# Performance work log

Hardware: AMD Instinct MI355X
Metric: run time of the kernel (lower is better)

The kernel has to match this reference:

```python
import jax, jax.numpy as jnp
import numpy as np

N = 50000
E = 800000
D_IN = 128
HID = 128
LAT = 64
NEG_SLOPE = 0.2


def setup_inputs() -> dict:
    key = jax.random.key(0)
    ks = jax.random.split(key, 16)
    g = lambda k, shape: jax.random.normal(k, shape, dtype=jnp.float32) * (1.0 / np.sqrt(shape[0]))
    x = jax.random.normal(ks[0], (N, D_IN), dtype=jnp.float32)
    edge_index = jax.random.randint(ks[1], (2, E), 0, N, dtype=jnp.int64)
    return {
        "x": x,
        "edge_index": edge_index,
        # lin1: Linear(D_IN, HID)
        "lin1_w": g(ks[2], (D_IN, HID)),
        "lin1_b": jnp.zeros((HID,), jnp.float32),
        # conv1: GATConv((D_IN, D_IN) -> HID), heads=1
        "w1_src": g(ks[3], (D_IN, HID)),
        "w1_dst": g(ks[4], (D_IN, HID)),
        "a1_src": g(ks[5], (HID,)),
        "a1_dst": g(ks[6], (HID,)),
        "b1": jnp.zeros((HID,), jnp.float32),
        # conv2: GATConv((HID, HID) -> LAT), heads=1
        "w2_src": g(ks[7], (HID, LAT)),
        "w2_dst": g(ks[8], (HID, LAT)),
        "a2_src": g(ks[9], (LAT,)),
        "a2_dst": g(ks[10], (LAT,)),
        "b2": jnp.zeros((LAT,), jnp.float32),
    }


def _gat_conv(x, src, dst, w_src, w_dst, a_src, a_dst, b):
    """PyG GATConv, heads=1, add_self_loops=False. x: [N, Din]."""
    n = x.shape[0]
    hs = x @ w_src                    # [N, C] messages (source transform)
    hd = x @ w_dst                    # [N, C] destination transform
    alpha_s = hs @ a_src              # [N]
    alpha_d = hd @ a_dst              # [N]
    e = jax.nn.leaky_relu(alpha_s[src] + alpha_d[dst], NEG_SLOPE)  # [E]
    # segment softmax over incoming edges per destination node
    m = jax.ops.segment_max(e, dst, num_segments=n)
    ex = jnp.exp(e - m[dst])
    denom = jax.ops.segment_sum(ex, dst, num_segments=n)
    alpha = ex / (denom[dst] + 1e-16)                              # [E]
    msg = hs[src] * alpha[:, None]                                 # [E, C]
    out = jax.ops.segment_sum(msg, dst, num_segments=n)            # [N, C]
    return out + b


def reference(x, edge_index, lin1_w, lin1_b, w1_src, w1_dst, a1_src, a1_dst, b1,
              w2_src, w2_dst, a2_src, a2_dst, b2):
    src, dst = edge_index[0], edge_index[1]
    z = _gat_conv(x, src, dst, w1_src, w1_dst, a1_src, a1_dst, b1)
    z = jax.nn.relu(z + x @ lin1_w + lin1_b)
    z = _gat_conv(z, src, dst, w2_src, w2_dst, a2_src, a2_dst, b2)
    return z
```

## Files before the change

kernel.cpp:

```cpp
#include <hip/hip_runtime.h>

static constexpr int N_NODES = 50000;
static constexpr int N_EDGES = 800000;
static constexpr int NPART = 8;
static constexpr int PART_SZ = N_NODES / NPART;

typedef __attribute__((ext_vector_type(8))) short bf16x8;
typedef __attribute__((ext_vector_type(4))) float f32x4;

__device__ __forceinline__ float bf2f(unsigned short u) {
  union { unsigned int i; float f; } v; v.i = ((unsigned int)u) << 16; return v.f;
}
__device__ __forceinline__ unsigned short f2bf(float f) {
  union { unsigned int i; float f; } v; v.f = f;
  unsigned int r = (v.i + 0x7fffu + ((v.i >> 16) & 1u)) >> 16;
  return (unsigned short)r;
}
__device__ __forceinline__ int clampN(int v) {
  unsigned u = (unsigned)v; return (u < (unsigned)N_NODES) ? (int)u : 0;
}

__global__ void k_detect(const int* __restrict__ ei, int* __restrict__ flag) {
  if (threadIdx.x == 0 && blockIdx.x == 0) {
    int z = ei[1] | ei[3] | ei[5] | ei[7];
    *flag = (z == 0) ? 1 : 0;
  }
}

__global__ void k_zero_out(float* __restrict__ out, int n) {
  int i = blockIdx.x * 256 + threadIdx.x;
  if (i < n) out[i] = 0.f;
}

__global__ void k_compact(const int* __restrict__ ei, const int* __restrict__ flag,
                          int* __restrict__ s32, int* __restrict__ d32) {
  int e = blockIdx.x * 256 + threadIdx.x;
  if (e < N_EDGES) {
    int f = *flag;
    s32[e] = clampN(ei[(size_t)e << f]);
    d32[e] = clampN(ei[(size_t)(N_EDGES + e) << f]);
  }
}

__global__ void k_prepw(const float* __restrict__ w1_src, const float* __restrict__ wlin,
                        const float* __restrict__ w2_src,
                        const float* __restrict__ w1_dst, const float* __restrict__ a1_dst,
                        const float* __restrict__ w2_dst, const float* __restrict__ a2_dst,
                        unsigned short* __restrict__ w1T, unsigned short* __restrict__ w2T,
                        float* __restrict__ c1dst, float* __restrict__ c2dst) {
  int idx = blockIdx.x * 256 + threadIdx.x;
  if (idx < 256 * 128) {
    int c = idx >> 7, k = idx & 127;
    float v = (c < 128) ? w1_src[k * 128 + c] : wlin[k * 128 + (c - 128)];
    w1T[idx] = f2bf(v);
  } else if (idx < 256 * 128 + 64 * 128) {
    int r = idx - 256 * 128;
    int c = r >> 7, k = r & 127;
    w2T[r] = f2bf(w2_src[k * 64 + c]);
  } else if (blockIdx.x == 160) {
    int k = threadIdx.x;
    if (k < 128) {
      float s1 = 0.f;
      for (int c = 0; c < 128; ++c) s1 += w1_dst[k * 128 + c] * a1_dst[c];
      c1dst[k] = s1;
      float s2 = 0.f;
      for (int c = 0; c < 64; ++c) s2 += w2_dst[k * 64 + c] * a2_dst[c];
      c2dst[k] = s2;
    }
  }
}

__global__ __launch_bounds__(256) void k_gemm1(
    const float* __restrict__ x, const unsigned short* __restrict__ w1T,
    const float* __restrict__ lin_b, const float* __restrict__ a1_src,
    const float* __restrict__ c1dst,
    unsigned short* __restrict__ hs1, unsigned short* __restrict__ linzb,
    float* __restrict__ as1, float* __restrict__ ad1) {
  int tid = threadIdx.x;
  int wv = tid >> 6, l = tid & 63;
  int lrow = l & 15, lk = l >> 4;
  int nb = blockIdx.x * 64 + wv * 16;
  int rowA = nb + lrow;
  int growA = rowA < N_NODES ? rowA : N_NODES - 1;
  bf16x8 afrag[4];
  float sd = 0.f;
#pragma unroll
  for (int ks = 0; ks < 4; ++ks) {
    const float* p = x + (size_t)growA * 128 + ks * 32 + lk * 8;
    float4 a0 = *(const float4*)p;
    float4 a1 = *(const float4*)(p + 4);
    bf16x8 af;
    af[0] = (short)f2bf(a0.x); af[1] = (short)f2bf(a0.y);
    af[2] = (short)f2bf(a0.z); af[3] = (short)f2bf(a0.w);
    af[4] = (short)f2bf(a1.x); af[5] = (short)f2bf(a1.y);
    af[6] = (short)f2bf(a1.z); af[7] = (short)f2bf(a1.w);
    afrag[ks] = af;
    int k0 = ks * 32 + lk * 8;
    float4 ca = *(const float4*)(c1dst + k0);
    float4 cb = *(const float4*)(c1dst + k0 + 4);
    sd += a0.x * ca.x + a0.y * ca.y + a0.z * ca.z + a0.w * ca.w +
          a1.x * cb.x + a1.y * cb.y + a1.z * cb.z + a1.w * cb.w;
  }
  sd += __shfl_xor(sd, 16, 64);
  sd += __shfl_xor(sd, 32, 64);
  if (lk == 0 && rowA < N_NODES) ad1[rowA] = sd;

  float pa[4] = {0.f, 0.f, 0.f, 0.f};
#pragma unroll
  for (int ch = 0; ch < 4; ++ch) {
    f32x4 acc[4] = {{0.f,0.f,0.f,0.f},{0.f,0.f,0.f,0.f},{0.f,0.f,0.f,0.f},{0.f,0.f,0.f,0.f}};
#pragma unroll
    for (int ks = 0; ks < 4; ++ks) {
      bf16x8 bfrag[4];
#pragma unroll
      for (int ct = 0; ct < 4; ++ct) {
        int col = ch * 64 + ct * 16 + lrow;
        bfrag[ct] = *(const bf16x8*)(w1T + (size_t)col * 128 + ks * 32 + lk * 8);
      }
#pragma unroll
      for (int ct = 0; ct < 4; ++ct)
        acc[ct] = __builtin_amdgcn_mfma_f32_16x16x32_bf16(afrag[ks], bfrag[ct], acc[ct], 0, 0, 0);
    }
#pragma unroll
    for (int ct = 0; ct < 4; ++ct) {
      int col = ch * 64 + ct * 16 + lrow;
      float av = (col < 128) ? a1_src[col] : 0.f;
      float bb = (col < 128) ? 0.f : lin_b[col - 128];
#pragma unroll
      for (int j = 0; j < 4; ++j) {
        int row = nb + lk * 4 + j;
        float v = acc[ct][j];
        if (row < N_NODES) {
          if (col < 128) hs1[(size_t)row * 128 + col] = f2bf(v);
          else linzb[(size_t)row * 128 + (col - 128)] = f2bf(v + bb);
        }
        if (col < 128) pa[j] += v * av;
      }
    }
  }
#pragma unroll
  for (int j = 0; j < 4; ++j) {
    pa[j] += __shfl_xor(pa[j], 1, 64);
    pa[j] += __shfl_xor(pa[j], 2, 64);
    pa[j] += __shfl_xor(pa[j], 4, 64);
    pa[j] += __shfl_xor(pa[j], 8, 64);
  }
  if (lrow == 0) {
#pragma unroll
    for (int j = 0; j < 4; ++j) {
      int row = nb + lk * 4 + j;
      if (row < N_NODES) as1[row] = pa[j];
    }
  }
}

__global__ __launch_bounds__(256) void k_gemm2(
    const unsigned short* __restrict__ zb, const unsigned short* __restrict__ w2T,
    const float* __restrict__ a2_src, const float* __restrict__ c2dst,
    unsigned short* __restrict__ hs2, float* __restrict__ as2, float* __restrict__ ad2) {
  int tid = threadIdx.x;
  int wv = tid >> 6, l = tid & 63;
  int lrow = l & 15, lk = l >> 4;
  int nb = blockIdx.x * 64 + wv * 16;
  int rowA = nb + lrow;
  int growA = rowA < N_NODES ? rowA : N_NODES - 1;
  bf16x8 afrag[4];
  float sd = 0.f;
#pragma unroll
  for (int ks = 0; ks < 4; ++ks) {
    bf16x8 af = *(const bf16x8*)(zb + (size_t)growA * 128 + ks * 32 + lk * 8);
    afrag[ks] = af;
    int k0 = ks * 32 + lk * 8;
    float4 ca = *(const float4*)(c2dst + k0);
    float4 cb = *(const float4*)(c2dst + k0 + 4);
    sd += bf2f((unsigned short)af[0]) * ca.x + bf2f((unsigned short)af[1]) * ca.y +
          bf2f((unsigned short)af[2]) * ca.z + bf2f((unsigned short)af[3]) * ca.w +
          bf2f((unsigned short)af[4]) * cb.x + bf2f((unsigned short)af[5]) * cb.y +
          bf2f((unsigned short)af[6]) * cb.z + bf2f((unsigned short)af[7]) * cb.w;
  }
  sd += __shfl_xor(sd, 16, 64);
  sd += __shfl_xor(sd, 32, 64);
  if (lk == 0 && rowA < N_NODES) ad2[rowA] = sd;

  f32x4 acc[4] = {{0.f,0.f,0.f,0.f},{0.f,0.f,0.f,0.f},{0.f,0.f,0.f,0.f},{0.f,0.f,0.f,0.f}};
#pragma unroll
  for (int ks = 0; ks < 4; ++ks) {
    bf16x8 bfrag[4];
#pragma unroll
    for (int ct = 0; ct < 4; ++ct) {
      int col = ct * 16 + lrow;
      bfrag[ct] = *(const bf16x8*)(w2T + (size_t)col * 128 + ks * 32 + lk * 8);
    }
#pragma unroll
    for (int ct = 0; ct < 4; ++ct)
      acc[ct] = __builtin_amdgcn_mfma_f32_16x16x32_bf16(afrag[ks], bfrag[ct], acc[ct], 0, 0, 0);
  }
  float pa[4] = {0.f, 0.f, 0.f, 0.f};
#pragma unroll
  for (int ct = 0; ct < 4; ++ct) {
    int col = ct * 16 + lrow;
    float av = a2_src[col];
#pragma unroll
    for (int j = 0; j < 4; ++j) {
      int row = nb + lk * 4 + j;
      if (row < N_NODES) hs2[(size_t)row * 64 + col] = f2bf(acc[ct][j]);
      pa[j] += acc[ct][j] * av;
    }
  }
#pragma unroll
  for (int j = 0; j < 4; ++j) {
    pa[j] += __shfl_xor(pa[j], 1, 64);
    pa[j] += __shfl_xor(pa[j], 2, 64);
    pa[j] += __shfl_xor(pa[j], 4, 64);
    pa[j] += __shfl_xor(pa[j], 8, 64);
  }
  if (lrow == 0) {
#pragma unroll
    for (int j = 0; j < 4; ++j) {
      int row = nb + lk * 4 + j;
      if (row < N_NODES) as2[row] = pa[j];
    }
  }
}

__global__ void k_count(const int* __restrict__ d32, int* __restrict__ deg) {
  int part = blockIdx.x & (NPART - 1);
  int e = (blockIdx.x >> 3) * 256 + threadIdx.x;
  if (e < N_EDGES) {
    int d = d32[e];
    int lo = part * PART_SZ;
    if (d >= lo && d < lo + PART_SZ) atomicAdd(&deg[d], 1);
  }
}

__global__ __launch_bounds__(256) void k_scan1(const int* __restrict__ deg,
                                               int* __restrict__ offs,
                                               int* __restrict__ bsums, int n) {
  __shared__ int wsum[4];
  int i = blockIdx.x * 256 + threadIdx.x;
  int lane = threadIdx.x & 63, wid = threadIdx.x >> 6;
  int v = (i < n) ? deg[i] : 0;
  int s = v;
#pragma unroll
  for (int o = 1; o < 64; o <<= 1) { int t = __shfl_up(s, o, 64); if (lane >= o) s += t; }
  if (lane == 63) wsum[wid] = s;
  __syncthreads();
  if (threadIdx.x == 0) {
    int a = 0;
#pragma unroll
    for (int w = 0; w < 4; ++w) { a += wsum[w]; wsum[w] = a; }
  }
  __syncthreads();
  int base = (wid > 0) ? wsum[wid - 1] : 0;
  if (i < n) offs[i] = base + s - v;
  if (threadIdx.x == 0) bsums[blockIdx.x] = wsum[3];
}

__global__ __launch_bounds__(256) void k_scan2(int* __restrict__ bsums, int nb,
                                               int* __restrict__ offs, int n, int etot) {
  __shared__ int wsum[4];
  int tid = threadIdx.x, lane = tid & 63, wid = tid >> 6;
  int v = (tid < nb) ? bsums[tid] : 0;
  int s = v;
#pragma unroll
  for (int o = 1; o < 64; o <<= 1) { int t = __shfl_up(s, o, 64); if (lane >= o) s += t; }
  if (lane == 63) wsum[wid] = s;
  __syncthreads();
  if (tid == 0) {
    int a = 0;
#pragma unroll
    for (int w = 0; w < 4; ++w) { a += wsum[w]; wsum[w] = a; }
  }
  __syncthreads();
  int base = (wid > 0) ? wsum[wid - 1] : 0;
  if (tid < nb) bsums[tid] = base + s - v;
  if (tid == 0) offs[n] = etot;
}

__global__ __launch_bounds__(256) void k_scan3(int* __restrict__ offs, int* __restrict__ cursor,
                                               const int* __restrict__ bsums, int n) {
  int i = blockIdx.x * 256 + threadIdx.x;
  if (i < n) {
    int o = offs[i] + bsums[blockIdx.x];
    offs[i] = o;
    cursor[i] = o;
  }
}

__global__ void k_fill(const int* __restrict__ s32, const int* __restrict__ d32,
                       int* __restrict__ cursor, int* __restrict__ ssrc) {
  int part = blockIdx.x & (NPART - 1);
  int e = (blockIdx.x >> 3) * 256 + threadIdx.x;
  if (e < N_EDGES) {
    int d = d32[e];
    int lo = part * PART_SZ;
    if (d >= lo && d < lo + PART_SZ) {
      int p = atomicAdd(&cursor[d], 1);
      if ((unsigned)p < (unsigned)N_EDGES) ssrc[p] = s32[e];
    }
  }
}

__global__ __launch_bounds__(256) void k_agg1(
    const int* __restrict__ offs, const int* __restrict__ ssrc,
    const float* __restrict__ as_, const float* __restrict__ ad_,
    const unsigned short* __restrict__ hs1, const float* __restrict__ b1,
    unsigned short* __restrict__ linzb) {
  int node = (int)((blockIdx.x * 256 + threadIdx.x) >> 6);
  if (node >= N_NODES) return;
  int lane = threadIdx.x & 63;
  int g = lane >> 4, cl = lane & 15;
  int o0 = offs[node], o1 = offs[node + 1];
  if (!((unsigned)o0 <= (unsigned)N_EDGES && (unsigned)o1 <= (unsigned)N_EDGES && o0 <= o1))
    { o0 = 0; o1 = 0; }
  int deg = o1 - o0;
  float ad = ad_[node];
  float acc[8];
#pragma unroll
  for (int k = 0; k < 8; ++k) acc[k] = 0.f;
  float ssum = 0.f;
  for (int j = g; j < deg; j += 4) {
    int s = clampN(ssrc[o0 + j]);
    float e = as_[s] + ad;
    e = e > 0.f ? e : 0.2f * e;
    float w = __expf(e);
    uint4 hv = *(const uint4*)(hs1 + (size_t)s * 128 + cl * 8);
    ssum += w;
    acc[0] += w * __uint_as_float(hv.x << 16);
    acc[1] += w * __uint_as_float(hv.x & 0xffff0000u);
    acc[2] += w * __uint_as_float(hv.y << 16);
    acc[3] += w * __uint_as_float(hv.y & 0xffff0000u);
    acc[4] += w * __uint_as_float(hv.z << 16);
    acc[5] += w * __uint_as_float(hv.z & 0xffff0000u);
    acc[6] += w * __uint_as_float(hv.w << 16);
    acc[7] += w * __uint_as_float(hv.w & 0xffff0000u);
  }
  ssum += __shfl_xor(ssum, 16, 64);
  ssum += __shfl_xor(ssum, 32, 64);
#pragma unroll
  for (int k = 0; k < 8; ++k) {
    acc[k] += __shfl_xor(acc[k], 16, 64);
    acc[k] += __shfl_xor(acc[k], 32, 64);
  }
  if (g == 0) {
    float inv = 1.f / (ssum + 1e-16f);
    uint4 lv = *(const uint4*)(linzb + (size_t)node * 128 + cl * 8);
    float4 ba = *(const float4*)(b1 + cl * 8);
    float4 bb = *(const float4*)(b1 + cl * 8 + 4);
    float z[8];
    z[0] = acc[0] * inv + ba.x + __uint_as_float(lv.x << 16);
    z[1] = acc[1] * inv + ba.y + __uint_as_float(lv.x & 0xffff0000u);
    z[2] = acc[2] * inv + ba.z + __uint_as_float(lv.y << 16);
    z[3] = acc[3] * inv + ba.w + __uint_as_float(lv.y & 0xffff0000u);
    z[4] = acc[4] * inv + bb.x + __uint_as_float(lv.z << 16);
    z[5] = acc[5] * inv + bb.y + __uint_as_float(lv.z & 0xffff0000u);
    z[6] = acc[6] * inv + bb.z + __uint_as_float(lv.w << 16);
    z[7] = acc[7] * inv + bb.w + __uint_as_float(lv.w & 0xffff0000u);
#pragma unroll
    for (int k = 0; k < 8; ++k) z[k] = z[k] > 0.f ? z[k] : 0.f;
    uint4 ov;
    ov.x = (unsigned)f2bf(z[0]) | ((unsigned)f2bf(z[1]) << 16);
    ov.y = (unsigned)f2bf(z[2]) | ((unsigned)f2bf(z[3]) << 16);
    ov.z = (unsigned)f2bf(z[4]) | ((unsigned)f2bf(z[5]) << 16);
    ov.w = (unsigned)f2bf(z[6]) | ((unsigned)f2bf(z[7]) << 16);
    *(uint4*)(linzb + (size_t)node * 128 + cl * 8) = ov;
  }
}

__global__ __launch_bounds__(256) void k_agg2(
    const int* __restrict__ offs, const int* __restrict__ ssrc,
    const float* __restrict__ as_, const float* __restrict__ ad_,
    const unsigned short* __restrict__ hs2, const float* __restrict__ b2,
    float* __restrict__ out) {
  int node = (int)((blockIdx.x * 256 + threadIdx.x) >> 6);
  if (node >= N_NODES) return;
  int lane = threadIdx.x & 63;
  int g = lane >> 3, cl = lane & 7;
  int o0 = offs[node], o1 = offs[node + 1];
  if (!((unsigned)o0 <= (unsigned)N_EDGES && (unsigned)o1 <= (unsigned)N_EDGES && o0 <= o1))
    { o0 = 0; o1 = 0; }
  int deg = o1 - o0;
  float ad = ad_[node];
  float acc[8];
#pragma unroll
  for (int k = 0; k < 8; ++k) acc[k] = 0.f;
  float ssum = 0.f;
  for (int j = g; j < deg; j += 8) {
    int s = clampN(ssrc[o0 + j]);
    float e = as_[s] + ad;
    e = e > 0.f ? e : 0.2f * e;
    float w = __expf(e);
    uint4 hv = *(const uint4*)(hs2 + (size_t)s * 64 + cl * 8);
    ssum += w;
    acc[0] += w * __uint_as_float(hv.x << 16);
    acc[1] += w * __uint_as_float(hv.x & 0xffff0000u);
    acc[2] += w * __uint_as_float(hv.y << 16);
    acc[3] += w * __uint_as_float(hv.y & 0xffff0000u);
    acc[4] += w * __uint_as_float(hv.z << 16);
    acc[5] += w * __uint_as_float(hv.z & 0xffff0000u);
    acc[6] += w * __uint_as_float(hv.w << 16);
    acc[7] += w * __uint_as_float(hv.w & 0xffff0000u);
  }
  ssum += __shfl_xor(ssum, 8, 64);
  ssum += __shfl_xor(ssum, 16, 64);
  ssum += __shfl_xor(ssum, 32, 64);
#pragma unroll
  for (int k = 0; k < 8; ++k) {
    acc[k] += __shfl_xor(acc[k], 8, 64);
    acc[k] += __shfl_xor(acc[k], 16, 64);
    acc[k] += __shfl_xor(acc[k], 32, 64);
  }
  if (g == 0) {
    float inv = 1.f / (ssum + 1e-16f);
    float4 ba = *(const float4*)(b2 + cl * 8);
    float4 bb = *(const float4*)(b2 + cl * 8 + 4);
    float4 oa, ob;
    oa.x = acc[0] * inv + ba.x;
    oa.y = acc[1] * inv + ba.y;
    oa.z = acc[2] * inv + ba.z;
    oa.w = acc[3] * inv + ba.w;
    ob.x = acc[4] * inv + bb.x;
    ob.y = acc[5] * inv + bb.y;
    ob.z = acc[6] * inv + bb.z;
    ob.w = acc[7] * inv + bb.w;
    *(float4*)(out + (size_t)node * 64 + cl * 8) = oa;
    *(float4*)(out + (size_t)node * 64 + cl * 8 + 4) = ob;
  }
}

extern "C" void kernel_launch(void* const* d_in, const int* in_sizes, int n_in,
                              void* d_out, int out_size, void* d_ws, size_t ws_size,
                              hipStream_t stream) {
  (void)in_sizes; (void)n_in;
  const float* x      = (const float*)d_in[0];
  const int*   ei     = (const int*)d_in[1];
  const float* lin1_w = (const float*)d_in[2];
  const float* lin1_b = (const float*)d_in[3];
  const float* w1_src = (const float*)d_in[4];
  const float* w1_dst = (const float*)d_in[5];
  const float* a1_src = (const float*)d_in[6];
  const float* a1_dst = (const float*)d_in[7];
  const float* b1     = (const float*)d_in[8];
  const float* w2_src = (const float*)d_in[9];
  const float* w2_dst = (const float*)d_in[10];
  const float* a2_src = (const float*)d_in[11];
  const float* a2_dst = (const float*)d_in[12];
  const float* b2     = (const float*)d_in[13];
  float* out = (float*)d_out;

  char* ws = (char*)d_ws;
  size_t off = 0;
  auto alloc = [&](size_t bytes) -> void* {
    void* p = ws + off;
    off += (bytes + 255) & ~(size_t)255;
    return p;
  };
  int* flag    = (int*)alloc(256);
  float* c1dst = (float*)alloc(128 * 4);
  float* c2dst = (float*)alloc(128 * 4);
  unsigned short* w1T = (unsigned short*)alloc(256 * 128 * 2);
  unsigned short* w2T = (unsigned short*)alloc(64 * 128 * 2);
  int* deg     = (int*)alloc((size_t)N_NODES * 4);
  int* offs    = (int*)alloc((size_t)(N_NODES + 1) * 4);
  int* cursor  = (int*)alloc((size_t)N_NODES * 4);
  int* bsums   = (int*)alloc(1024);
  float* as1   = (float*)alloc((size_t)N_NODES * 4);
  float* ad1   = (float*)alloc((size_t)N_NODES * 4);
  float* as2   = (float*)alloc((size_t)N_NODES * 4);
  float* ad2   = (float*)alloc((size_t)N_NODES * 4);
  int* s32     = (int*)alloc((size_t)N_EDGES * 4);
  int* d32     = (int*)alloc((size_t)N_EDGES * 4);
  int* ssrc    = (int*)alloc((size_t)N_EDGES * 4);
  unsigned short* hs1   = (unsigned short*)alloc((size_t)N_NODES * 128 * 2);
  unsigned short* hs2   = (unsigned short*)alloc((size_t)N_NODES * 64 * 2);
  unsigned short* linzb = (unsigned short*)alloc((size_t)N_NODES * 128 * 2);

  if (off > ws_size) {
    k_zero_out<<<(out_size + 255) / 256, 256, 0, stream>>>(out, out_size);
    return;
  }

  int ebl  = (N_EDGES + 255) / 256;
  int ebl8 = NPART * ebl;
  int nbl  = (N_NODES + 3) / 4;
  int gbl  = (N_NODES + 63) / 64;
  hipMemsetAsync(deg, 0, (size_t)N_NODES * 4, stream);
  k_detect<<<1, 64, 0, stream>>>(ei, flag);
  k_prepw<<<161, 256, 0, stream>>>(w1_src, lin1_w, w2_src, w1_dst, a1_dst, w2_dst, a2_dst,
                                   w1T, w2T, c1dst, c2dst);
  k_compact<<<ebl, 256, 0, stream>>>(ei, flag, s32, d32);
  k_gemm1<<<gbl, 256, 0, stream>>>(x, w1T, lin1_b, a1_src, c1dst, hs1, linzb, as1, ad1);
  k_count<<<ebl8, 256, 0, stream>>>(d32, deg);
  int nb = (N_NODES + 255) / 256;
  k_scan1<<<nb, 256, 0, stream>>>(deg, offs, bsums, N_NODES);
  k_scan2<<<1, 256, 0, stream>>>(bsums, nb, offs, N_NODES, N_EDGES);
  k_scan3<<<nb, 256, 0, stream>>>(offs, cursor, bsums, N_NODES);
  k_fill<<<ebl8, 256, 0, stream>>>(s32, d32, cursor, ssrc);
  k_agg1<<<nbl, 256, 0, stream>>>(offs, ssrc, as1, ad1, hs1, b1, linzb);
  k_gemm2<<<gbl, 256, 0, stream>>>(linzb, w2T, a2_src, c2dst, hs2, as2, ad2);
  k_agg2<<<nbl, 256, 0, stream>>>(offs, ssrc, as2, ad2, hs2, b2, out);
}
```

Baseline: 222.8 us.

## Restructure GEMM kernels to keep weights in registers and vectorize stores

Splits the first GEMM into a conversion pass (x to bf16 plus the destination-attention dot), a persistent GEMM where each wave holds its 64-column weight slice in registers and loops over row tiles, and a separate pass that computes the source attention scalar from hs1. The second GEMM also preloads weights and uses swapped MFMA operands so each lane stores four contiguous bf16 outputs. The aim is to stop reloading weight fragments per chunk and to replace scattered 2-byte stores with packed stores. In exchange it adds two extra kernel launches and an extra round trip of x and hs1 through memory, and it aliases several buffers into one shared workspace region to save space.

```diff
diff --git a/kernel.cpp b/kernel.cpp
--- a/kernel.cpp
+++ b/kernel.cpp
@@ -4,6 +4,7 @@
 static constexpr int N_EDGES = 800000;
 static constexpr int NPART = 8;
 static constexpr int PART_SZ = N_NODES / NPART;
+static constexpr int NTILES = N_NODES / 16;
 
 typedef __attribute__((ext_vector_type(8))) short bf16x8;
 typedef __attribute__((ext_vector_type(4))) float f32x4;
@@ -70,88 +71,102 @@
   }
 }
 
+__global__ __launch_bounds__(256) void k_prepx(
+    const float* __restrict__ x, const float* __restrict__ c1dst,
+    unsigned short* __restrict__ xb, float* __restrict__ ad1) {
+  int gid = blockIdx.x * 256 + threadIdx.x;
+  int row = gid >> 4, sl = gid & 15;
+  const float* p = x + (size_t)row * 128 + sl * 8;
+  float4 a0 = *(const float4*)p;
+  float4 a1 = *(const float4*)(p + 4);
+  uint4 o;
+  o.x = (unsigned)f2bf(a0.x) | ((unsigned)f2bf(a0.y) << 16);
+  o.y = (unsigned)f2bf(a0.z) | ((unsigned)f2bf(a0.w) << 16);
+  o.z = (unsigned)f2bf(a1.x) | ((unsigned)f2bf(a1.y) << 16);
+  o.w = (unsigned)f2bf(a1.z) | ((unsigned)f2bf(a1.w) << 16);
+  *(uint4*)(xb + (size_t)row * 128 + sl * 8) = o;
+  float4 ca = *(const float4*)(c1dst + sl * 8);
+  float4 cb = *(const float4*)(c1dst + sl * 8 + 4);
+  float sd = a0.x * ca.x + a0.y * ca.y + a0.z * ca.z + a0.w * ca.w +
+             a1.x * cb.x + a1.y * cb.y + a1.z * cb.z + a1.w * cb.w;
+  sd += __shfl_xor(sd, 1, 64);
+  sd += __shfl_xor(sd, 2, 64);
+  sd += __shfl_xor(sd, 4, 64);
+  sd += __shfl_xor(sd, 8, 64);
+  if (sl == 0) ad1[row] = sd;
+}
+
 __global__ __launch_bounds__(256) void k_gemm1(
-    const float* __restrict__ x, const unsigned short* __restrict__ w1T,
-    const float* __restrict__ lin_b, const float* __restrict__ a1_src,
-    const float* __restrict__ c1dst,
-    unsigned short* __restrict__ hs1, unsigned short* __restrict__ linzb,
-    float* __restrict__ as1, float* __restrict__ ad1) {
+    const unsigned short* __restrict__ xb, const unsigned short* __restrict__ w1T,
+    const float* __restrict__ lin_b,
+    unsigned short* __restrict__ hs1, unsigned short* __restrict__ linzb) {
   int tid = threadIdx.x;
   int wv = tid >> 6, l = tid & 63;
   int lrow = l & 15, lk = l >> 4;
-  int nb = blockIdx.x * 64 + wv * 16;
-  int rowA = nb + lrow;
-  int growA = rowA < N_NODES ? rowA : N_NODES - 1;
-  bf16x8 afrag[4];
-  float sd = 0.f;
-#pragma unroll
-  for (int ks = 0; ks < 4; ++ks) {
-    const float* p = x + (size_t)growA * 128 + ks * 32 + lk * 8;
-    float4 a0 = *(const float4*)p;
-    float4 a1 = *(const float4*)(p + 4);
-    bf16x8 af;
-    af[0] = (short)f2bf(a0.x); af[1] = (short)f2bf(a0.y);
-    af[2] = (short)f2bf(a0.z); af[3] = (short)f2bf(a0.w);
-    af[4] = (short)f2bf(a1.x); af[5] = (short)f2bf(a1.y);
-    af[6] = (short)f2bf(a1.z); af[7] = (short)f2bf(a1.w);
-    afrag[ks] = af;
-    int k0 = ks * 32 + lk * 8;
-    float4 ca = *(const float4*)(c1dst + k0);
-    float4 cb = *(const float4*)(c1dst + k0 + 4);
-    sd += a0.x * ca.x + a0.y * ca.y + a0.z * ca.z + a0.w * ca.w +
-          a1.x * cb.x + a1.y * cb.y + a1.z * cb.z + a1.w * cb.w;
-  }
-  sd += __shfl_xor(sd, 16, 64);
-  sd += __shfl_xor(sd, 32, 64);
-  if (lk == 0 && rowA < N_NODES) ad1[rowA] = sd;
-
-  float pa[4] = {0.f, 0.f, 0.f, 0.f};
-#pragma unroll
-  for (int ch = 0; ch < 4; ++ch) {
+  int cb = wv * 64;
+  bf16x8 wfrag[4][4];
+#pragma unroll
+  for (int ct = 0; ct < 4; ++ct)
+#pragma unroll
+    for (int ks = 0; ks < 4; ++ks)
+      wfrag[ct][ks] = *(const bf16x8*)(w1T + (size_t)(cb + ct * 16 + lrow) * 128 + ks * 32 + lk * 8);
+  for (int t = blockIdx.x; t < NTILES; t += gridDim.x) {
+    int row = t * 16 + lrow;
+    bf16x8 xfrag[4];
+#pragma unroll
+    for (int ks = 0; ks < 4; ++ks)
+      xfrag[ks] = *(const bf16x8*)(xb + (size_t)row * 128 + ks * 32 + lk * 8);
     f32x4 acc[4] = {{0.f,0.f,0.f,0.f},{0.f,0.f,0.f,0.f},{0.f,0.f,0.f,0.f},{0.f,0.f,0.f,0.f}};
 #pragma unroll
-    for (int ks = 0; ks < 4; ++ks) {
-      bf16x8 bfrag[4];
+    for (int ks = 0; ks < 4; ++ks)
+#pragma unroll
+      for (int ct = 0; ct < 4; ++ct)
+        acc[ct] = __builtin_amdgcn_mfma_f32_16x16x32_bf16(wfrag[ct][ks], xfrag[ks], acc[ct], 0, 0, 0);
+    if (cb < 128) {
 #pragma unroll
       for (int ct = 0; ct < 4; ++ct) {
-        int col = ch * 64 + ct * 16 + lrow;
-        bfrag[ct] = *(const bf16x8*)(w1T + (size_t)col * 128 + ks * 32 + lk * 8);
+        int col0 = cb + ct * 16 + lk * 4;
+        uint2 pv;
+        pv.x = (unsigned)f2bf(acc[ct][0]) | ((unsigned)f2bf(acc[ct][1]) << 16);
+        pv.y = (unsigned)f2bf(acc[ct][2]) | ((unsigned)f2bf(acc[ct][3]) << 16);
+        *(uint2*)(hs1 + (size_t)row * 128 + col0) = pv;
       }
-#pragma unroll
-      for (int ct = 0; ct < 4; ++ct)
-        acc[ct] = __builtin_amdgcn_mfma_f32_16x16x32_bf16(afrag[ks], bfrag[ct], acc[ct], 0, 0, 0);
-    }
-#pragma unroll
-    for (int ct = 0; ct < 4; ++ct) {
-      int col = ch * 64 + ct * 16 + lrow;
-      float av = (col < 128) ? a1_src[col] : 0.f;
-      float bb = (col < 128) ? 0.f : lin_b[col - 128];
-#pragma unroll
-      for (int j = 0; j < 4; ++j) {
-        int row = nb + lk * 4 + j;
-        float v = acc[ct][j];
-        if (row < N_NODES) {
-          if (col < 128) hs1[(size_t)row * 128 + col] = f2bf(v);
-          else linzb[(size_t)row * 128 + (col - 128)] = f2bf(v + bb);
-        }
-        if (col < 128) pa[j] += v * av;
+    } else {
+#pragma unroll
+      for (int ct = 0; ct < 4; ++ct) {
+        int col0 = cb - 128 + ct * 16 + lk * 4;
+        float4 bv = *(const float4*)(lin_b + col0);
+        uint2 pv;
+        pv.x = (unsigned)f2bf(acc[ct][0] + bv.x) | ((unsigned)f2bf(acc[ct][1] + bv.y) << 16);
+        pv.y = (unsigned)f2bf(acc[ct][2] + bv.z) | ((unsigned)f2bf(acc[ct][3] + bv.w) << 16);
+        *(uint2*)(linzb + (size_t)row * 128 + col0) = pv;
       }
     }
   }
-#pragma unroll
-  for (int j = 0; j < 4; ++j) {
-    pa[j] += __shfl_xor(pa[j], 1, 64);
-    pa[j] += __shfl_xor(pa[j], 2, 64);
-    pa[j] += __shfl_xor(pa[j], 4, 64);
-    pa[j] += __shfl_xor(pa[j], 8, 64);
-  }
-  if (lrow == 0) {
-#pragma unroll
-    for (int j = 0; j < 4; ++j) {
-      int row = nb + lk * 4 + j;
-      if (row < N_NODES) as1[row] = pa[j];
-    }
-  }
+}
+
+__global__ __launch_bounds__(256) void k_alpha1(
+    const unsigned short* __restrict__ hs1, const float* __restrict__ a1_src,
+    float* __restrict__ as1) {
+  int gid = blockIdx.x * 256 + threadIdx.x;
+  int node = gid >> 3, s = gid & 7;
+  if (node >= N_NODES) return;
+  uint4 h0 = *(const uint4*)(hs1 + (size_t)node * 128 + s * 16);
+  uint4 h1 = *(const uint4*)(hs1 + (size_t)node * 128 + s * 16 + 8);
+  const float* a = a1_src + s * 16;
+  float sa =
+    bf2f((unsigned short)(h0.x & 0xffffu)) * a[0] + bf2f((unsigned short)(h0.x >> 16)) * a[1] +
+    bf2f((unsigned short)(h0.y & 0xffffu)) * a[2] + bf2f((unsigned short)(h0.y >> 16)) * a[3] +
+    bf2f((unsigned short)(h0.z & 0xffffu)) * a[4] + bf2f((unsigned short)(h0.z >> 16)) * a[5] +
+    bf2f((unsigned short)(h0.w & 0xffffu)) * a[6] + bf2f((unsigned short)(h0.w >> 16)) * a[7] +
+    bf2f((unsigned short)(h1.x & 0xffffu)) * a[8] + bf2f((unsigned short)(h1.x >> 16)) * a[9] +
+    bf2f((unsigned short)(h1.y & 0xffffu)) * a[10] + bf2f((unsigned short)(h1.y >> 16)) * a[11] +
+    bf2f((unsigned short)(h1.z & 0xffffu)) * a[12] + bf2f((unsigned short)(h1.z >> 16)) * a[13] +
+    bf2f((unsigned short)(h1.w & 0xffffu)) * a[14] + bf2f((unsigned short)(h1.w >> 16)) * a[15];
+  sa += __shfl_xor(sa, 1, 64);
+  sa += __shfl_xor(sa, 2, 64);
+  sa += __shfl_xor(sa, 4, 64);
+  if (s == 0) as1[node] = sa;
 }
 
 __global__ __launch_bounds__(256) void k_gemm2(
@@ -161,15 +176,21 @@
   int tid = threadIdx.x;
   int wv = tid >> 6, l = tid & 63;
   int lrow = l & 15, lk = l >> 4;
-  int nb = blockIdx.x * 64 + wv * 16;
-  int rowA = nb + lrow;
-  int growA = rowA < N_NODES ? rowA : N_NODES - 1;
-  bf16x8 afrag[4];
+  int g = blockIdx.x * 4 + wv;
+  if (g >= NTILES) return;
+  bf16x8 wfrag[4][4];
+#pragma unroll
+  for (int ct = 0; ct < 4; ++ct)
+#pragma unroll
+    for (int ks = 0; ks < 4; ++ks)
+      wfrag[ct][ks] = *(const bf16x8*)(w2T + (size_t)(ct * 16 + lrow) * 128 + ks * 32 + lk * 8);
+  int row = g * 16 + lrow;
+  bf16x8 xfrag[4];
   float sd = 0.f;
 #pragma unroll
   for (int ks = 0; ks < 4; ++ks) {
-    bf16x8 af = *(const bf16x8*)(zb + (size_t)growA * 128 + ks * 32 + lk * 8);
-    afrag[ks] = af;
+    bf16x8 af = *(const bf16x8*)(zb + (size_t)row * 128 + ks * 32 + lk * 8);
+    xfrag[ks] = af;
     int k0 = ks * 32 + lk * 8;
     float4 ca = *(const float4*)(c2dst + k0);
     float4 cb = *(const float4*)(c2dst + k0 + 4);
@@ -180,47 +201,28 @@
   }
   sd += __shfl_xor(sd, 16, 64);
   sd += __shfl_xor(sd, 32, 64);
-  if (lk == 0 && rowA < N_NODES) ad2[rowA] = sd;
+  if (lk == 0) ad2[row] = sd;
 
   f32x4 acc[4] = {{0.f,0.f,0.f,0.f},{0.f,0.f,0.f,0.f},{0.f,0.f,0.f,0.f},{0.f,0.f,0.f,0.f}};
 #pragma unroll
-  for (int ks = 0; ks < 4; ++ks) {
-    bf16x8 bfrag[4];
-#pragma unroll
-    for (int ct = 0; ct < 4; ++ct) {
-      int col = ct * 16 + lrow;
-      bfrag[ct] = *(const bf16x8*)(w2T + (size_t)col * 128 + ks * 32 + lk * 8);
-    }
+  for (int ks = 0; ks < 4; ++ks)
 #pragma unroll
     for (int ct = 0; ct < 4; ++ct)
-      acc[ct] = __builtin_amdgcn_mfma_f32_16x16x32_bf16(afrag[ks], bfrag[ct], acc[ct], 0, 0, 0);
-  }
-  float pa[4] = {0.f, 0.f, 0.f, 0.f};
+      acc[ct] = __builtin_amdgcn_mfma_f32_16x16x32_bf16(wfrag[ct][ks], xfrag[ks], acc[ct], 0, 0, 0);
+  float pa = 0.f;
 #pragma unroll
   for (int ct = 0; ct < 4; ++ct) {
-    int col = ct * 16 + lrow;
-    float av = a2_src[col];
-#pragma unroll
-    for (int j = 0; j < 4; ++j) {
-      int row = nb + lk * 4 + j;
-      if (row < N_NODES) hs2[(size_t)row * 64 + col] = f2bf(acc[ct][j]);
-      pa[j] += acc[ct][j] * av;
-    }
-  }
-#pragma unroll
-  for (int j = 0; j < 4; ++j) {
-    pa[j] += __shfl_xor(pa[j], 1, 64);
-    pa[j] += __shfl_xor(pa[j], 2, 64);
-    pa[j] += __shfl_xor(pa[j], 4, 64);
-    pa[j] += __shfl_xor(pa[j], 8, 64);
-  }
-  if (lrow == 0) {
-#pragma unroll
-    for (int j = 0; j < 4; ++j) {
-      int row = nb + lk * 4 + j;
-      if (row < N_NODES) as2[row] = pa[j];
-    }
-  }
+    int col0 = ct * 16 + lk * 4;
+    float4 av = *(const float4*)(a2_src + col0);
+    pa += acc[ct][0] * av.x + acc[ct][1] * av.y + acc[ct][2] * av.z + acc[ct][3] * av.w;
+    uint2 pv;
+    pv.x = (unsigned)f2bf(acc[ct][0]) | ((unsigned)f2bf(acc[ct][1]) << 16);
+    pv.y = (unsigned)f2bf(acc[ct][2]) | ((unsigned)f2bf(acc[ct][3]) << 16);
+    *(uint2*)(hs2 + (size_t)row * 64 + col0) = pv;
+  }
+  pa += __shfl_xor(pa, 16, 64);
+  pa += __shfl_xor(pa, 32, 64);
+  if (lk == 0) as2[row] = pa;
 }
 
 __global__ void k_count(const int* __restrict__ d32, int* __restrict__ deg) {
@@ -466,14 +468,16 @@
   int* bsums   = (int*)alloc(1024);
   float* as1   = (float*)alloc((size_t)N_NODES * 4);
   float* ad1   = (float*)alloc((size_t)N_NODES * 4);
-  float* as2   = (float*)alloc((size_t)N_NODES * 4);
-  float* ad2   = (float*)alloc((size_t)N_NODES * 4);
   int* s32     = (int*)alloc((size_t)N_EDGES * 4);
   int* d32     = (int*)alloc((size_t)N_EDGES * 4);
-  int* ssrc    = (int*)alloc((size_t)N_EDGES * 4);
   unsigned short* hs1   = (unsigned short*)alloc((size_t)N_NODES * 128 * 2);
-  unsigned short* hs2   = (unsigned short*)alloc((size_t)N_NODES * 64 * 2);
   unsigned short* linzb = (unsigned short*)alloc((size_t)N_NODES * 128 * 2);
+  char* U = (char*)alloc((size_t)N_NODES * 128 * 2);
+  unsigned short* xb  = (unsigned short*)U;
+  int* ssrc           = (int*)U;
+  unsigned short* hs2 = (unsigned short*)(U + (size_t)N_EDGES * 4);
+  float* as2          = (float*)(U + (size_t)N_EDGES * 4 + (size_t)N_NODES * 128);
+  float* ad2          = (float*)(U + (size_t)N_EDGES * 4 + (size_t)N_NODES * 128 + (size_t)N_NODES * 4);
 
   if (off > ws_size) {
     k_zero_out<<<(out_size + 255) / 256, 256, 0, stream>>>(out, out_size);
@@ -483,13 +487,14 @@
   int ebl  = (N_EDGES + 255) / 256;
   int ebl8 = NPART * ebl;
   int nbl  = (N_NODES + 3) / 4;
-  int gbl  = (N_NODES + 63) / 64;
   hipMemsetAsync(deg, 0, (size_t)N_NODES * 4, stream);
   k_detect<<<1, 64, 0, stream>>>(ei, flag);
   k_prepw<<<161, 256, 0, stream>>>(w1_src, lin1_w, w2_src, w1_dst, a1_dst, w2_dst, a2_dst,
                                    w1T, w2T, c1dst, c2dst);
   k_compact<<<ebl, 256, 0, stream>>>(ei, flag, s32, d32);
-  k_gemm1<<<gbl, 256, 0, stream>>>(x, w1T, lin1_b, a1_src, c1dst, hs1, linzb, as1, ad1);
+  k_prepx<<<NTILES, 256, 0, stream>>>(x, c1dst, xb, ad1);
+  k_gemm1<<<1024, 256, 0, stream>>>(xb, w1T, lin1_b, hs1, linzb);
+  k_alpha1<<<(N_NODES * 8 + 255) / 256, 256, 0, stream>>>(hs1, a1_src, as1);
   k_count<<<ebl8, 256, 0, stream>>>(d32, deg);
   int nb = (N_NODES + 255) / 256;
   k_scan1<<<nb, 256, 0, stream>>>(deg, offs, bsums, N_NODES);
@@ -497,6 +502,6 @@
   k_scan3<<<nb, 256, 0, stream>>>(offs, cursor, bsums, N_NODES);
   k_fill<<<ebl8, 256, 0, stream>>>(s32, d32, cursor, ssrc);
   k_agg1<<<nbl, 256, 0, stream>>>(offs, ssrc, as1, ad1, hs1, b1, linzb);
-  k_gemm2<<<gbl, 256, 0, stream>>>(linzb, w2T, a2_src, c2dst, hs2, as2, ad2);
+  k_gemm2<<<(NTILES + 3) / 4, 256, 0, stream>>>(linzb, w2T, a2_src, c2dst, hs2, as2, ad2);
   k_agg2<<<nbl, 256, 0, stream>>>(offs, ssrc, as2, ad2, hs2, b2, out);
 }
```

After: 209.7 us. 5.9% less time.
